# Kernel tuning notes

Hardware: AMD Instinct MI355X
Metric: run time of the kernel (lower is better)

## Reference

```python
import jax, jax.numpy as jnp
import numpy as np
from jax import lax

SUBSAMPLE = 2

def _grect(b, bs):
    # grid rect (inclusive) for int boxes b [N,4]
    return jnp.stack([b[:, 0] // bs, b[:, 1] // bs,
                      (b[:, 2] - 1) // bs, (b[:, 3] - 1) // bs], axis=1)

def _rect_overlap(r, allr):
    # r [N,4], allr [M,4] inclusive grid rects -> [N,M] bool
    return ((r[:, None, 0] <= allr[None, :, 2]) & (allr[None, :, 0] <= r[:, None, 2]) &
            (r[:, None, 1] <= allr[None, :, 3]) & (allr[None, :, 1] <= r[:, None, 3]))

def _forward(boxes_curr, boxes_prev, H, W, HG, WG, bs):
    S = SUBSAMPLE
    Nc, Np = boxes_curr.shape[0], boxes_prev.shape[0]
    Hs, Ws = H // S, W // S
    oc, sc = boxes_curr[:, :4], boxes_curr[:, 4]
    op, sp = boxes_prev[:, :4], boxes_prev[:, 4]
    ic = oc.astype(jnp.int32)            # original int coords
    ip = op.astype(jnp.int32)
    cc = (oc / S).astype(jnp.int32)      # subsampled int coords
    cp = (op / S).astype(jnp.int32)

    # --- pairwise IoU on subsampled boxes (matches get_iou semantics) ---
    a = cc.astype(jnp.float32); b = cp.astype(jnp.float32)
    ix1 = jnp.maximum(a[:, None, 0], b[None, :, 0])
    iy1 = jnp.maximum(a[:, None, 1], b[None, :, 1])
    ix2 = jnp.minimum(a[:, None, 2], b[None, :, 2])
    iy2 = jnp.minimum(a[:, None, 3], b[None, :, 3])
    inter = jnp.clip(ix2 - ix1, 0.0) * jnp.clip(iy2 - iy1, 0.0)
    areaA = (a[:, 2] - a[:, 0]) * (a[:, 3] - a[:, 1])
    areaB = (b[:, 2] - b[:, 0]) * (b[:, 3] - b[:, 1])
    iou = inter / (areaA[:, None] + areaB[None, :] - inter)
    best_iou = jnp.max(iou, axis=1)
    best_j = jnp.argmax(iou, axis=1)     # first max, matches strict '>' loop
    matched = best_iou > 0.0
    ig = 1.0 - best_iou

    # --- grid rects & isolation test ---
    gc, gp = _grect(ic, bs), _grect(ip, bs)
    gpj = gp[best_j]
    union = jnp.stack([jnp.minimum(gc[:, 0], gpj[:, 0]), jnp.minimum(gc[:, 1], gpj[:, 1]),
                       jnp.maximum(gc[:, 2], gpj[:, 2]), jnp.maximum(gc[:, 3], gpj[:, 3])], 1)
    wrect = jnp.where(matched[:, None], union, gc)
    allr = jnp.concatenate([gc, gp], 0)                      # [Nc+Np,4]
    cover_other = _rect_overlap(gc, allr) | (matched[:, None] & _rect_overlap(gpj, allr))
    kk = jnp.arange(Nc + Np)[None, :]
    excl = (kk == jnp.arange(Nc)[:, None]) | (matched[:, None] & (kk == Nc + best_j[:, None]))
    isolated = ~jnp.any(cover_other & ~excl, axis=1)

    big = (ic[:, 3] - ic[:, 1]) >= 100
    val_c = jnp.where(isolated & big & (sc >= 0.7), 2.0, 1.0)
    matched_prev = jnp.any(matched[:, None] & (best_j[:, None] == jnp.arange(Np)[None, :]), axis=0)

    rects_w = jnp.concatenate([wrect, gp], 0)
    vals_w = jnp.concatenate([val_c, jnp.ones((Np,), val_c.dtype)], 0)
    act_w = jnp.concatenate([jnp.ones((Nc,), bool), ~matched_prev], 0)
    yy, xx = jnp.arange(HG), jnp.arange(WG)
    ry = (yy[None, :] >= rects_w[:, 1:2]) & (yy[None, :] <= rects_w[:, 3:4])   # [Nw,HG]
    rx = (xx[None, :] >= rects_w[:, 0:1]) & (xx[None, :] <= rects_w[:, 2:3])   # [Nw,WG]
    cover = act_w[:, None, None] & ry[:, :, None] & rx[:, None, :]
    order = jnp.arange(rects_w.shape[0])
    last = jnp.max(jnp.where(cover, order[:, None, None], -1), axis=0)
    grid_ig = jnp.where(last >= 0, vals_w[jnp.clip(last, 0)], 0.0)[None, None]  # [1,1,HG,WG]

    # --- subsampled mask: scatter-max rect writes (order-independent) ---
    rects_m = jnp.concatenate([cc, cp[best_j], cp], 0)
    vals_m = jnp.concatenate([ig * sc, ig * sp[best_j], sp], 0)
    act_m = jnp.concatenate([jnp.ones((Nc,)), matched.astype(jnp.float32),
                             (~matched_prev).astype(jnp.float32)], 0)
    ys, xs = jnp.arange(Hs), jnp.arange(Ws)
    def step(m, w):
        r, v, a = w
        row = (ys >= r[1]) & (ys < r[3])
        col = (xs >= r[0]) & (xs < r[2])
        m = jnp.maximum(m, jnp.where(row[:, None] & col[None, :], v * a, 0.0))
        return m, None
    m0 = jnp.zeros((Hs, Ws), jnp.float32)
    m, _ = lax.scan(step, m0, (rects_m, vals_m, act_m))
    mask = jnp.repeat(jnp.repeat(m, SUBSAMPLE, axis=0), SUBSAMPLE, axis=1)[None, None]  # nearest x2
    return mask, grid_ig

def setup_inputs() -> dict:
    H, W, HG, WG, bs = 2048, 4096, 16, 32, 128
    def make_boxes(key, n, max_w=400.0, max_h=300.0):
        k1, k2, k3, k4, k5 = jax.random.split(key, 5)
        x1 = jax.random.uniform(k1, (n,), minval=0.0, maxval=W - max_w - 1)
        y1 = jax.random.uniform(k2, (n,), minval=0.0, maxval=H - max_h - 1)
        bw = jax.random.uniform(k3, (n,), minval=8.0, maxval=max_w)
        bh = jax.random.uniform(k4, (n,), minval=8.0, maxval=max_h)
        sc = jax.random.uniform(k5, (n,))
        return jnp.stack([x1, y1, x1 + bw, y1 + bh, sc], axis=1).astype(jnp.float32)
    key = jax.random.key(0)
    kc, kp = jax.random.split(key)
    return {"boxes_curr": make_boxes(kc, 512), "boxes_prev": make_boxes(kp, 512),
            "H": H, "W": W, "HG": HG, "WG": WG, "block_size": bs}

def reference(boxes_curr, boxes_prev, H, W, HG, WG, block_size):
    return _forward(boxes_curr, boxes_prev, H, W, HG, WG, block_size)
```

## Files before the change

### kernel.cpp

```cpp
#include <hip/hip_runtime.h>

constexpr int H  = 2048, W = 4096, HG = 16, WG = 32, BS = 128;
constexpr int S  = 2, Hs = H / S, Ws = W / S;
constexpr int TILE_R = 32, TILE_C = 64;
constexpr int LMAX = 1536;

__global__ __launch_bounds__(64) void k_match(
    const float* __restrict__ bc, const float* __restrict__ bp,
    int Nc, int Np,
    int* __restrict__ wrect, float* __restrict__ val_c,
    int* __restrict__ bj_matched,
    int* __restrict__ rm, float* __restrict__ wm)
{
    int i = blockIdx.x, lane = threadIdx.x;
    float x1 = bc[i*5+0], y1 = bc[i*5+1], x2 = bc[i*5+2], y2 = bc[i*5+3], sc = bc[i*5+4];
    float ax1 = (float)(int)(x1*0.5f), ay1 = (float)(int)(y1*0.5f);
    float ax2 = (float)(int)(x2*0.5f), ay2 = (float)(int)(y2*0.5f);
    float areaA = (ax2-ax1)*(ay2-ay1);

    float bi = -1.0f; int bj = 0;
    for (int j = lane; j < Np; j += 64) {
        float px1 = bp[j*5+0], py1 = bp[j*5+1], px2 = bp[j*5+2], py2 = bp[j*5+3];
        float bx1 = (float)(int)(px1*0.5f), by1 = (float)(int)(py1*0.5f);
        float bx2 = (float)(int)(px2*0.5f), by2 = (float)(int)(py2*0.5f);
        float ix1 = fmaxf(ax1,bx1), iy1 = fmaxf(ay1,by1);
        float ix2 = fminf(ax2,bx2), iy2 = fminf(ay2,by2);
        float inter = fmaxf(ix2-ix1,0.0f)*fmaxf(iy2-iy1,0.0f);
        float areaB = (bx2-bx1)*(by2-by1);
        float iou = inter/(areaA+areaB-inter);
        if (iou > bi || (iou == bi && j < bj)) { bi = iou; bj = j; }
    }
    for (int off = 32; off; off >>= 1) {
        float oi = __shfl_xor(bi, off);
        int   oj = __shfl_xor(bj, off);
        if (oi > bi || (oi == bi && oj < bj)) { bi = oi; bj = oj; }
    }
    bool m = bi > 0.0f;

    int gx1=(int)x1/BS, gy1=(int)y1/BS, gx2=((int)x2-1)/BS, gy2=((int)y2-1)/BS;
    float pjx1=bp[bj*5+0], pjy1=bp[bj*5+1], pjx2=bp[bj*5+2], pjy2=bp[bj*5+3], spj=bp[bj*5+4];
    int hx1=(int)pjx1/BS, hy1=(int)pjy1/BS, hx2=((int)pjx2-1)/BS, hy2=((int)pjy2-1)/BS;

    bool bad = false;
    int NT = Nc + Np;
    for (int k = lane; k < NT; k += 64) {
        const float* q = (k < Nc) ? &bc[(size_t)k*5] : &bp[(size_t)(k-Nc)*5];
        int qx1=(int)q[0]/BS, qy1=(int)q[1]/BS, qx2=((int)q[2]-1)/BS, qy2=((int)q[3]-1)/BS;
        bool ov = (gx1<=qx2)&&(qx1<=gx2)&&(gy1<=qy2)&&(qy1<=gy2);
        if (m) ov = ov || ((hx1<=qx2)&&(qx1<=hx2)&&(hy1<=qy2)&&(qy1<=hy2));
        bool excl = (k == i) || (m && k == Nc + bj);
        bad |= (ov && !excl);
    }
    bool anybad = __any(bad);

    if (lane == 0) {
        bool big = ((int)y2 - (int)y1) >= 100;
        val_c[i] = (!anybad && big && sc >= 0.7f) ? 2.0f : 1.0f;
        int4 wr = make_int4(gx1,gy1,gx2,gy2);
        if (m) { wr.x=min(gx1,hx1); wr.y=min(gy1,hy1); wr.z=max(gx2,hx2); wr.w=max(gy2,hy2); }
        ((int4*)wrect)[i] = wr;
        bj_matched[i] = m ? bj : -1;
        float ig = 1.0f - bi;
        ((int4*)rm)[i] = make_int4((int)(x1*0.5f),(int)(y1*0.5f),(int)(x2*0.5f),(int)(y2*0.5f));
        wm[i] = ig * sc;
        ((int4*)rm)[Nc+i] = make_int4((int)(pjx1*0.5f),(int)(pjy1*0.5f),(int)(pjx2*0.5f),(int)(pjy2*0.5f));
        wm[Nc+i] = m ? ig * spj : 0.0f;
    }
}

__global__ __launch_bounds__(256) void k_gridmask(
    const float* __restrict__ bp,
    const int* __restrict__ rm, const float* __restrict__ wm,
    const int* __restrict__ wrect, const float* __restrict__ val_c,
    const int* __restrict__ bj_matched,
    int Nc, int Np, float* __restrict__ out)
{
    __shared__ int4  Lr[LMAX];
    __shared__ float Lw[LMAX];
    __shared__ unsigned int bits[64];
    __shared__ int cnt, glast;
    int tid = threadIdx.x;
    if (tid == 0) { cnt = 0; glast = -1; }
    if (tid < 64) bits[tid] = 0u;
    __syncthreads();

    for (int i = tid; i < Nc; i += 256) {
        int bj = bj_matched[i];
        if (bj >= 0) atomicOr(&bits[bj >> 5], 1u << (bj & 31));
    }
    __syncthreads();

    int bx = blockIdx.x * TILE_C;
    int by = blockIdx.y * TILE_R;

    for (int r = tid; r < 2*Nc; r += 256) {
        int4 q = ((const int4*)rm)[r];
        float w = wm[r];
        if (w > 0.0f && q.x < bx+TILE_C && q.z > bx && q.y < by+TILE_R && q.w > by) {
            int idx = atomicAdd(&cnt, 1);
            Lr[idx] = q; Lw[idx] = w;
        }
    }
    for (int j = tid; j < Np; j += 256) {
        bool mp = (bits[j >> 5] >> (j & 31)) & 1u;
        if (!mp) {
            float w = bp[j*5+4];
            if (w > 0.0f) {
                int4 q = make_int4((int)(bp[j*5+0]*0.5f),(int)(bp[j*5+1]*0.5f),
                                   (int)(bp[j*5+2]*0.5f),(int)(bp[j*5+3]*0.5f));
                if (q.x < bx+TILE_C && q.z > bx && q.y < by+TILE_R && q.w > by) {
                    int idx = atomicAdd(&cnt, 1);
                    Lr[idx] = q; Lw[idx] = w;
                }
            }
        }
    }

    int cell = blockIdx.y * gridDim.x + blockIdx.x;
    int last = -1;
    if (cell < HG*WG) {
        int gy = cell / WG, gx = cell % WG;
        int NT = Nc + Np;
        for (int r = tid; r < NT; r += 256) {
            int4 q; bool act;
            if (r < Nc) { q = ((const int4*)wrect)[r]; act = true; }
            else {
                int j = r - Nc;
                act = !((bits[j >> 5] >> (j & 31)) & 1u);
                q = make_int4((int)bp[j*5+0]/BS, (int)bp[j*5+1]/BS,
                              ((int)bp[j*5+2]-1)/BS, ((int)bp[j*5+3]-1)/BS);
            }
            if (act && gx >= q.x && gx <= q.z && gy >= q.y && gy <= q.w) last = r;
        }
        if (last >= 0) atomicMax(&glast, last);
    }
    __syncthreads();

    if (cell < HG*WG && tid == 0) {
        int g = glast;
        out[(size_t)H*W + cell] = (g >= 0) ? (g < Nc ? val_c[g] : 1.0f) : 0.0f;
    }

    int n = cnt;
    int tx = tid & 31;
    int ty = tid >> 5;
    int c0 = bx + tx * 2;
    int r0 = by + ty * 4;
    float mv[4][2];
    #pragma unroll
    for (int rr = 0; rr < 4; rr++) { mv[rr][0] = 0.0f; mv[rr][1] = 0.0f; }
    for (int k = 0; k < n; k++) {
        int4 q = Lr[k];
        float w = Lw[k];
        bool cx0 = (c0     >= q.x) && (c0     < q.z);
        bool cx1 = (c0 + 1 >= q.x) && (c0 + 1 < q.z);
        #pragma unroll
        for (int rr = 0; rr < 4; rr++) {
            int y = r0 + rr;
            bool cy = (y >= q.y) && (y < q.w);
            if (cy && cx0) mv[rr][0] = fmaxf(mv[rr][0], w);
            if (cy && cx1) mv[rr][1] = fmaxf(mv[rr][1], w);
        }
    }
    #pragma unroll
    for (int rr = 0; rr < 4; rr++) {
        int y = r0 + rr;
        float4 v = make_float4(mv[rr][0], mv[rr][0], mv[rr][1], mv[rr][1]);
        *(float4*)&out[(size_t)(2*y)     * W + 2*c0] = v;
        *(float4*)&out[(size_t)(2*y + 1) * W + 2*c0] = v;
    }
}

extern "C" void kernel_launch(void* const* d_in, const int* in_sizes, int n_in,
                              void* d_out, int out_size, void* d_ws, size_t ws_size,
                              hipStream_t stream)
{
    const float* bc = (const float*)d_in[0];
    const float* bp = (const float*)d_in[1];
    int Nc = in_sizes[0] / 5;
    int Np = in_sizes[1] / 5;
    float* out = (float*)d_out;

    int* w = (int*)d_ws;
    int* wrect      = w;          w += Nc * 4;
    float* val_c    = (float*)w;  w += Nc;
    int* bj_matched = w;          w += Nc;
    int* rm         = w;          w += 2 * Nc * 4;
    float* wm       = (float*)w;  w += 2 * Nc;

    k_match<<<Nc, 64, 0, stream>>>(bc, bp, Nc, Np, wrect, val_c, bj_matched, rm, wm);
    dim3 gmask(Ws / TILE_C, Hs / TILE_R);
    k_gridmask<<<gmask, 256, 0, stream>>>(bp, rm, wm, wrect, val_c, bj_matched, Nc, Np, out);
}
```

Measured before the change: 27.66 us.

## Fuse match and grid-mask kernels into one persistent kernel with ticket queue

Merges the per-box matching kernel and the mask/grid kernel into a single launch. Blocks first pull current-box indices from an atomic ticket counter and do each match with 256 threads, then spin on a global done counter before building the mask tiles. This removes one kernel launch and the gap between launches. It adds a memset, a global spin barrier that relies on all 1024 blocks being co-resident or on work draining first, and the bits array shrinks to 16 words, which limits Np to 512.

Measured after the change: 110.6 us. +299.8%, slower.

```diff
diff --git a/kernel.cpp b/kernel.cpp
--- a/kernel.cpp
+++ b/kernel.cpp
@@ -4,84 +4,106 @@
 constexpr int S  = 2, Hs = H / S, Ws = W / S;
 constexpr int TILE_R = 32, TILE_C = 64;
 constexpr int LMAX = 1536;
-
-__global__ __launch_bounds__(64) void k_match(
+constexpr int NB  = (Ws / TILE_C) * (Hs / TILE_R);
+
+__global__ __launch_bounds__(256) void k_fused(
     const float* __restrict__ bc, const float* __restrict__ bp,
     int Nc, int Np,
+    int* __restrict__ ticket, int* __restrict__ done,
     int* __restrict__ wrect, float* __restrict__ val_c,
-    int* __restrict__ bj_matched,
-    int* __restrict__ rm, float* __restrict__ wm)
-{
-    int i = blockIdx.x, lane = threadIdx.x;
-    float x1 = bc[i*5+0], y1 = bc[i*5+1], x2 = bc[i*5+2], y2 = bc[i*5+3], sc = bc[i*5+4];
-    float ax1 = (float)(int)(x1*0.5f), ay1 = (float)(int)(y1*0.5f);
-    float ax2 = (float)(int)(x2*0.5f), ay2 = (float)(int)(y2*0.5f);
-    float areaA = (ax2-ax1)*(ay2-ay1);
-
-    float bi = -1.0f; int bj = 0;
-    for (int j = lane; j < Np; j += 64) {
-        float px1 = bp[j*5+0], py1 = bp[j*5+1], px2 = bp[j*5+2], py2 = bp[j*5+3];
-        float bx1 = (float)(int)(px1*0.5f), by1 = (float)(int)(py1*0.5f);
-        float bx2 = (float)(int)(px2*0.5f), by2 = (float)(int)(py2*0.5f);
-        float ix1 = fmaxf(ax1,bx1), iy1 = fmaxf(ay1,by1);
-        float ix2 = fminf(ax2,bx2), iy2 = fminf(ay2,by2);
-        float inter = fmaxf(ix2-ix1,0.0f)*fmaxf(iy2-iy1,0.0f);
-        float areaB = (bx2-bx1)*(by2-by1);
-        float iou = inter/(areaA+areaB-inter);
-        if (iou > bi || (iou == bi && j < bj)) { bi = iou; bj = j; }
-    }
-    for (int off = 32; off; off >>= 1) {
-        float oi = __shfl_xor(bi, off);
-        int   oj = __shfl_xor(bj, off);
-        if (oi > bi || (oi == bi && oj < bj)) { bi = oi; bj = oj; }
-    }
-    bool m = bi > 0.0f;
-
-    int gx1=(int)x1/BS, gy1=(int)y1/BS, gx2=((int)x2-1)/BS, gy2=((int)y2-1)/BS;
-    float pjx1=bp[bj*5+0], pjy1=bp[bj*5+1], pjx2=bp[bj*5+2], pjy2=bp[bj*5+3], spj=bp[bj*5+4];
-    int hx1=(int)pjx1/BS, hy1=(int)pjy1/BS, hx2=((int)pjx2-1)/BS, hy2=((int)pjy2-1)/BS;
-
-    bool bad = false;
-    int NT = Nc + Np;
-    for (int k = lane; k < NT; k += 64) {
-        const float* q = (k < Nc) ? &bc[(size_t)k*5] : &bp[(size_t)(k-Nc)*5];
-        int qx1=(int)q[0]/BS, qy1=(int)q[1]/BS, qx2=((int)q[2]-1)/BS, qy2=((int)q[3]-1)/BS;
-        bool ov = (gx1<=qx2)&&(qx1<=gx2)&&(gy1<=qy2)&&(qy1<=gy2);
-        if (m) ov = ov || ((hx1<=qx2)&&(qx1<=hx2)&&(hy1<=qy2)&&(qy1<=hy2));
-        bool excl = (k == i) || (m && k == Nc + bj);
-        bad |= (ov && !excl);
-    }
-    bool anybad = __any(bad);
-
-    if (lane == 0) {
-        bool big = ((int)y2 - (int)y1) >= 100;
-        val_c[i] = (!anybad && big && sc >= 0.7f) ? 2.0f : 1.0f;
-        int4 wr = make_int4(gx1,gy1,gx2,gy2);
-        if (m) { wr.x=min(gx1,hx1); wr.y=min(gy1,hy1); wr.z=max(gx2,hx2); wr.w=max(gy2,hy2); }
-        ((int4*)wrect)[i] = wr;
-        bj_matched[i] = m ? bj : -1;
-        float ig = 1.0f - bi;
-        ((int4*)rm)[i] = make_int4((int)(x1*0.5f),(int)(y1*0.5f),(int)(x2*0.5f),(int)(y2*0.5f));
-        wm[i] = ig * sc;
-        ((int4*)rm)[Nc+i] = make_int4((int)(pjx1*0.5f),(int)(pjy1*0.5f),(int)(pjx2*0.5f),(int)(pjy2*0.5f));
-        wm[Nc+i] = m ? ig * spj : 0.0f;
-    }
-}
-
-__global__ __launch_bounds__(256) void k_gridmask(
-    const float* __restrict__ bp,
-    const int* __restrict__ rm, const float* __restrict__ wm,
-    const int* __restrict__ wrect, const float* __restrict__ val_c,
-    const int* __restrict__ bj_matched,
-    int Nc, int Np, float* __restrict__ out)
+    int* __restrict__ bj_matched, int* __restrict__ rm, float* __restrict__ wm,
+    float* __restrict__ out)
 {
     __shared__ int4  Lr[LMAX];
     __shared__ float Lw[LMAX];
-    __shared__ unsigned int bits[64];
-    __shared__ int cnt, glast;
-    int tid = threadIdx.x;
-    if (tid == 0) { cnt = 0; glast = -1; }
-    if (tid < 64) bits[tid] = 0u;
+    __shared__ unsigned int bits[16];
+    __shared__ int sh_t, cnt, glast, s_iso;
+    __shared__ float red_f[4];
+    __shared__ int   red_j[4];
+
+    int tid  = threadIdx.x;
+    int lane = tid & 63, wv = tid >> 6;
+
+    for (;;) {
+        __syncthreads();
+        if (tid == 0) sh_t = atomicAdd(ticket, 1);
+        __syncthreads();
+        int i = sh_t;
+        if (i >= Nc) break;
+
+        float x1 = bc[i*5+0], y1 = bc[i*5+1], x2 = bc[i*5+2], y2 = bc[i*5+3], sc = bc[i*5+4];
+        float ax1 = (float)(int)(x1*0.5f), ay1 = (float)(int)(y1*0.5f);
+        float ax2 = (float)(int)(x2*0.5f), ay2 = (float)(int)(y2*0.5f);
+        float areaA = (ax2-ax1)*(ay2-ay1);
+
+        float bi = -1.0f; int bj = 0;
+        for (int j = tid; j < Np; j += 256) {
+            float bx1 = (float)(int)(bp[j*5+0]*0.5f), by1 = (float)(int)(bp[j*5+1]*0.5f);
+            float bx2 = (float)(int)(bp[j*5+2]*0.5f), by2 = (float)(int)(bp[j*5+3]*0.5f);
+            float ix1 = fmaxf(ax1,bx1), iy1 = fmaxf(ay1,by1);
+            float ix2 = fminf(ax2,bx2), iy2 = fminf(ay2,by2);
+            float inter = fmaxf(ix2-ix1,0.0f)*fmaxf(iy2-iy1,0.0f);
+            float areaB = (bx2-bx1)*(by2-by1);
+            float iou = inter/(areaA+areaB-inter);
+            if (iou > bi || (iou == bi && j < bj)) { bi = iou; bj = j; }
+        }
+        #pragma unroll
+        for (int off = 32; off; off >>= 1) {
+            float oi = __shfl_xor(bi, off);
+            int   oj = __shfl_xor(bj, off);
+            if (oi > bi || (oi == bi && oj < bj)) { bi = oi; bj = oj; }
+        }
+        if (tid == 0) s_iso = 0;
+        if (lane == 0) { red_f[wv] = bi; red_j[wv] = bj; }
+        __syncthreads();
+        bi = red_f[0]; bj = red_j[0];
+        #pragma unroll
+        for (int w2 = 1; w2 < 4; w2++) {
+            float oi = red_f[w2]; int oj = red_j[w2];
+            if (oi > bi || (oi == bi && oj < bj)) { bi = oi; bj = oj; }
+        }
+        bool m = bi > 0.0f;
+
+        int gx1=(int)x1/BS, gy1=(int)y1/BS, gx2=((int)x2-1)/BS, gy2=((int)y2-1)/BS;
+        float pjx1=bp[bj*5+0], pjy1=bp[bj*5+1], pjx2=bp[bj*5+2], pjy2=bp[bj*5+3], spj=bp[bj*5+4];
+        int hx1=(int)pjx1/BS, hy1=(int)pjy1/BS, hx2=((int)pjx2-1)/BS, hy2=((int)pjy2-1)/BS;
+
+        bool bad = false;
+        int NT = Nc + Np;
+        for (int k = tid; k < NT; k += 256) {
+            const float* q = (k < Nc) ? &bc[(size_t)k*5] : &bp[(size_t)(k-Nc)*5];
+            int qx1=(int)q[0]/BS, qy1=(int)q[1]/BS, qx2=((int)q[2]-1)/BS, qy2=((int)q[3]-1)/BS;
+            bool ov = (gx1<=qx2)&&(qx1<=gx2)&&(gy1<=qy2)&&(qy1<=gy2);
+            if (m) ov = ov || ((hx1<=qx2)&&(qx1<=hx2)&&(hy1<=qy2)&&(qy1<=hy2));
+            bool excl = (k == i) || (m && k == Nc + bj);
+            bad |= (ov && !excl);
+        }
+        if (__any(bad) && lane == 0) atomicOr(&s_iso, 1);
+        __syncthreads();
+
+        if (tid == 0) {
+            bool big = ((int)y2 - (int)y1) >= 100;
+            val_c[i] = (!s_iso && big && sc >= 0.7f) ? 2.0f : 1.0f;
+            int4 wr = make_int4(gx1,gy1,gx2,gy2);
+            if (m) { wr.x=min(gx1,hx1); wr.y=min(gy1,hy1); wr.z=max(gx2,hx2); wr.w=max(gy2,hy2); }
+            ((int4*)wrect)[i] = wr;
+            bj_matched[i] = m ? bj : -1;
+            float ig = 1.0f - bi;
+            ((int4*)rm)[i] = make_int4((int)(x1*0.5f),(int)(y1*0.5f),(int)(x2*0.5f),(int)(y2*0.5f));
+            wm[i] = ig * sc;
+            ((int4*)rm)[Nc+i] = make_int4((int)(pjx1*0.5f),(int)(pjy1*0.5f),(int)(pjx2*0.5f),(int)(pjy2*0.5f));
+            wm[Nc+i] = m ? ig * spj : 0.0f;
+            __threadfence();
+            __hip_atomic_fetch_add(done, 1, __ATOMIC_RELEASE, __HIP_MEMORY_SCOPE_AGENT);
+        }
+    }
+
+    if (tid == 0) {
+        while (__hip_atomic_load(done, __ATOMIC_ACQUIRE, __HIP_MEMORY_SCOPE_AGENT) < Nc)
+            __builtin_amdgcn_s_sleep(4);
+        cnt = 0; glast = -1;
+    }
+    if (tid < 16) bits[tid] = 0u;
     __syncthreads();
 
     for (int i = tid; i < Nc; i += 256) {
@@ -90,8 +112,9 @@
     }
     __syncthreads();
 
-    int bx = blockIdx.x * TILE_C;
-    int by = blockIdx.y * TILE_R;
+    int tileb = blockIdx.x;
+    int bx = (tileb & 31) * TILE_C;
+    int by = (tileb >> 5) * TILE_R;
 
     for (int r = tid; r < 2*Nc; r += 256) {
         int4 q = ((const int4*)rm)[r];
@@ -116,10 +139,9 @@
         }
     }
 
-    int cell = blockIdx.y * gridDim.x + blockIdx.x;
     int last = -1;
-    if (cell < HG*WG) {
-        int gy = cell / WG, gx = cell % WG;
+    if (tileb < HG*WG) {
+        int gy = tileb / WG, gx = tileb % WG;
         int NT = Nc + Np;
         for (int r = tid; r < NT; r += 256) {
             int4 q; bool act;
@@ -136,9 +158,9 @@
     }
     __syncthreads();
 
-    if (cell < HG*WG && tid == 0) {
+    if (tileb < HG*WG && tid == 0) {
         int g = glast;
-        out[(size_t)H*W + cell] = (g >= 0) ? (g < Nc ? val_c[g] : 1.0f) : 0.0f;
+        out[(size_t)H*W + tileb] = (g >= 0) ? (g < Nc ? val_c[g] : 1.0f) : 0.0f;
     }
 
     int n = cnt;
@@ -181,14 +203,17 @@
     int Np = in_sizes[1] / 5;
     float* out = (float*)d_out;
 
-    int* w = (int*)d_ws;
+    int* ctr = (int*)d_ws;
+    int* ticket = ctr + 0;
+    int* done   = ctr + 1;
+    int* w = (int*)((char*)d_ws + 64);
     int* wrect      = w;          w += Nc * 4;
     float* val_c    = (float*)w;  w += Nc;
     int* bj_matched = w;          w += Nc;
     int* rm         = w;          w += 2 * Nc * 4;
     float* wm       = (float*)w;  w += 2 * Nc;
 
-    k_match<<<Nc, 64, 0, stream>>>(bc, bp, Nc, Np, wrect, val_c, bj_matched, rm, wm);
-    dim3 gmask(Ws / TILE_C, Hs / TILE_R);
-    k_gridmask<<<gmask, 256, 0, stream>>>(bp, rm, wm, wrect, val_c, bj_matched, Nc, Np, out);
+    hipMemsetAsync(ctr, 0, 16, stream);
+    k_fused<<<NB, 256, 0, stream>>>(bc, bp, Nc, Np, ticket, done,
+                                    wrect, val_c, bj_matched, rm, wm, out);
 }
```
